# Kernel tuning notes

Measured on AMD Instinct MI355X. Metric: run time of the kernel, lower is better.

The kernel has to match this reference:

```python
import jax, jax.numpy as jnp
import numpy as np

DT_MIN, DT_MAX, STAB_EPS, RMS_EPS = 1e-4, 10.0, 1e-8, 1e-6


def soft_clamp(x, mn=DT_MIN, mx=DT_MAX):
    center = (mx + mn) / 2.0
    half = (mx - mn) / 2.0
    return center + half * jnp.tanh((x - center) / half)


def setup_inputs() -> dict:
    key = jax.random.key(0)
    ks = jax.random.split(key, 8)
    B, L, D, N = 1, 4096, 1024, 16
    s = D ** -0.5
    x = jax.random.normal(ks[0], (B, L, D), jnp.float32)
    # S4D-real style init: A = -exp(A_log), rows = -(1..N)
    A_log = jnp.broadcast_to(jnp.log(jnp.arange(1, N + 1, dtype=jnp.float32)), (D, N))
    W_delta = jax.random.normal(ks[1], (D, D), jnp.float32) * s
    b_delta = jax.random.normal(ks[2], (D,), jnp.float32) * 0.1
    W_B = jax.random.normal(ks[3], (D, N), jnp.float32) * s
    W_C = jax.random.normal(ks[4], (D, N), jnp.float32) * s
    D_skip = jax.random.normal(ks[5], (D,), jnp.float32) * 0.1 + 1.0
    norm_weight = jnp.ones((D,), jnp.float32)
    return {"x": x, "A_log": A_log, "W_delta": W_delta, "b_delta": b_delta,
            "W_B": W_B, "W_C": W_C, "D_skip": D_skip, "norm_weight": norm_weight}


def reference(x, A_log, W_delta, b_delta, W_B, W_C, D_skip, norm_weight):
    # RMSNorm pre-norm
    rms = jnp.sqrt(jnp.mean(x * x, axis=-1, keepdims=True) + RMS_EPS)
    xn = norm_weight * x / rms                                  # (B, L, D)

    # input-dependent (selective) parameters
    delta = soft_clamp(jax.nn.softplus(xn @ W_delta + b_delta))  # (B, L, D)
    Bp = xn @ W_B                                               # (B, L, N)
    C = xn @ W_C                                                # (B, L, N)
    A = -jnp.exp(A_log)                                         # (D, N)

    # guarded Tustin (bilinear) discretization
    half_dA = 0.5 * delta[..., None] * A                        # (B, L, D, N)
    denom_inv = 1.0 / jnp.maximum(1.0 - half_dA, STAB_EPS)
    A_bar = (1.0 + half_dA) * denom_inv                         # (B, L, D, N)
    B_bar = jnp.sqrt(delta)[..., None] * Bp[:, :, None, :] * denom_inv
    Bx = B_bar * xn[..., None]                                  # (B, L, D, N)

    # linear recurrence h_t = A_bar_t * h_{t-1} + Bx_t ; y_t = sum_n C_t * h_t
    def step(h, inp):
        a_t, bx_t, c_t = inp
        h = a_t * h + bx_t                                      # (B, D, N)
        y_t = jnp.einsum('bdn,bn->bd', h, c_t)
        return h, y_t

    h0 = jnp.zeros((x.shape[0], A.shape[0], A.shape[1]), x.dtype)
    seq = (jnp.moveaxis(A_bar, 1, 0), jnp.moveaxis(Bx, 1, 0), jnp.moveaxis(C, 1, 0))
    _, ys = jax.lax.scan(step, h0, seq)
    y = jnp.moveaxis(ys, 0, 1) + D_skip * xn                    # skip connection
    return y
```

## Files before the change

kernel.cpp:

```cpp
#include <hip/hip_runtime.h>
#include <hip/hip_fp16.h>
#include <cmath>

typedef _Float16 half8 __attribute__((ext_vector_type(8)));
typedef _Float16 half4_t __attribute__((ext_vector_type(4)));
typedef float f32x4 __attribute__((ext_vector_type(4)));

#define LDIM 4096
#define DDIM 1024
#define NSTATE 16
#define NCHUNK 128
#define CLEN 32

#define GLD16(g, l) __builtin_amdgcn_global_load_lds( \
    (const __attribute__((address_space(1))) void*)(g), \
    (__attribute__((address_space(3))) void*)(l), 16, 0, 0)

__global__ __launch_bounds__(256) void k_prep_norm(const float* __restrict__ x,
                                                   const float* __restrict__ nw,
                                                   const float* __restrict__ W,
                                                   const float* __restrict__ WB,
                                                   const float* __restrict__ WC,
                                                   _Float16* __restrict__ xnh,
                                                   _Float16* __restrict__ Wt,
                                                   _Float16* __restrict__ BCe) {
  const int b = blockIdx.x, t = threadIdx.x;
  if (b < 4096) {
    const int l = b;
    float4 v = ((const float4*)(x + (size_t)l * DDIM))[t];
    float ss = v.x * v.x + v.y * v.y + v.z * v.z + v.w * v.w;
#pragma unroll
    for (int off = 32; off; off >>= 1) ss += __shfl_xor(ss, off, 64);
    __shared__ float sred[4];
    if ((t & 63) == 0) sred[t >> 6] = ss;
    __syncthreads();
    float tot = sred[0] + sred[1] + sred[2] + sred[3];
    float r = rsqrtf(tot * (1.0f / (float)DDIM) + 1e-6f);
    float4 wv = ((const float4*)nw)[t];
    half4_t h;
    h[0] = (_Float16)(v.x * wv.x * r); h[1] = (_Float16)(v.y * wv.y * r);
    h[2] = (_Float16)(v.z * wv.z * r); h[3] = (_Float16)(v.w * wv.w * r);
    ((half4_t*)(xnh + (size_t)l * DDIM))[t] = h;
  } else if (b < 4352) {
    __shared__ float tile[64][65];
    const int bb = b - 4096;
    const int n0 = (bb & 15) * 64, k0 = (bb >> 4) * 64;
#pragma unroll
    for (int i = 0; i < 16; ++i) {
      int idx = t + i * 256;
      int kk = idx >> 6, nn = idx & 63;
      tile[kk][nn] = W[(size_t)(k0 + kk) * DDIM + n0 + nn];
    }
    __syncthreads();
#pragma unroll
    for (int i = 0; i < 16; ++i) {
      int idx = t + i * 256;
      int nn = idx >> 6, kk = idx & 63;
      Wt[(size_t)(n0 + nn) * DDIM + k0 + kk] = (_Float16)tile[kk][nn];
    }
  } else {
    const int by2 = b - 4352;
#pragma unroll
    for (int rr = 0; rr < 2; ++rr) {
      int r = 2 * by2 + rr;
      const float* src = (r & 1) ? WC : WB;
      int n = r >> 1;
#pragma unroll
      for (int j = 0; j < 4; ++j) {
        int k = t * 4 + j;
        BCe[(size_t)r * DDIM + k] = (_Float16)src[(size_t)k * NSTATE + n];
      }
    }
  }
}

__global__ __launch_bounds__(256, 2) void k_gemm64(const _Float16* __restrict__ Ah,
                                                   const _Float16* __restrict__ Bh,
                                                   const _Float16* __restrict__ B2h,
                                                   const float* __restrict__ b_delta,
                                                   _Float16* __restrict__ sdh,
                                                   float* __restrict__ bpc) {
  __shared__ __align__(16) _Float16 As[2][128 * 64];
  __shared__ __align__(16) _Float16 Bs[2][64 * 64];
  __shared__ __align__(16) _Float16 B2s[2][32 * 64];
  const int t = threadIdx.x;
  const int w = t >> 6, lane = t & 63;
  const int quad = lane >> 4, l16 = lane & 15;
  const int wr = w >> 1, wc = w & 1;
  const int bid = blockIdx.x;
  const int bx = bid & 15, by = bid >> 4;
  const int tileM = by * 128, tileN = bx * 64;
  const int srow = lane >> 3;
  const int sslot = (lane & 7) ^ srow;
  const _Float16* gA0 = Ah + (size_t)(tileM + w * 32 + srow) * DDIM + sslot * 8;
  const _Float16* gB0 = Bh + (size_t)(tileN + w * 16 + srow) * DDIM + sslot * 8;
  const _Float16* gC0 = B2h + (size_t)(w * 8 + srow) * DDIM + sslot * 8;

  f32x4 acc[4][2], acc2[4];
#pragma unroll
  for (int i = 0; i < 4; ++i) {
    acc2[i] = (f32x4){0.f, 0.f, 0.f, 0.f};
#pragma unroll
    for (int j = 0; j < 2; ++j) acc[i][j] = (f32x4){0.f, 0.f, 0.f, 0.f};
  }

  auto stage = [&](int kt, int p) {
    const int ko = kt * 64;
#pragma unroll
    for (int g = 0; g < 4; ++g)
      GLD16(gA0 + (size_t)g * 8 * DDIM + ko, &As[p][(w * 32 + g * 8) * 64]);
#pragma unroll
    for (int g = 0; g < 2; ++g)
      GLD16(gB0 + (size_t)g * 8 * DDIM + ko, &Bs[p][(w * 16 + g * 8) * 64]);
    if (bx == 0)
      GLD16(gC0 + ko, &B2s[p][(w * 8) * 64]);
  };

  stage(0, 0);
  for (int kt = 0; kt < 16; ++kt) {
    const int p = kt & 1;
    __syncthreads();
    if (kt < 15) stage(kt + 1, p ^ 1);
#pragma unroll
    for (int ks = 0; ks < 2; ++ks) {
      const int sw = ((ks * 4 + quad) ^ (l16 & 7)) * 8;
      half8 af[4], bf[2];
#pragma unroll
      for (int i = 0; i < 4; ++i)
        af[i] = *(const half8*)&As[p][(wr * 64 + i * 16 + l16) * 64 + sw];
#pragma unroll
      for (int j = 0; j < 2; ++j)
        bf[j] = *(const half8*)&Bs[p][(wc * 32 + j * 16 + l16) * 64 + sw];
#pragma unroll
      for (int i = 0; i < 4; ++i)
#pragma unroll
        for (int j = 0; j < 2; ++j)
          acc[i][j] = __builtin_amdgcn_mfma_f32_16x16x32_f16(af[i], bf[j], acc[i][j], 0, 0, 0);
      if (bx == 0) {
        half8 cf = *(const half8*)&B2s[p][(wc * 16 + l16) * 64 + sw];
#pragma unroll
        for (int i = 0; i < 4; ++i)
          acc2[i] = __builtin_amdgcn_mfma_f32_16x16x32_f16(af[i], cf, acc2[i], 0, 0, 0);
      }
    }
  }

  const float cC = 5.00005f, cH = 4.99995f, invH = 1.0f / 4.99995f;
  float bdl[2];
#pragma unroll
  for (int j = 0; j < 2; ++j) bdl[j] = b_delta[tileN + wc * 32 + j * 16 + l16];
#pragma unroll
  for (int i = 0; i < 4; ++i) {
#pragma unroll
    for (int r = 0; r < 4; ++r) {
      int row = tileM + wr * 64 + i * 16 + quad * 4 + r;
#pragma unroll
      for (int j = 0; j < 2; ++j) {
        int col = tileN + wc * 32 + j * 16 + l16;
        float z = acc[i][j][r] + bdl[j];
        float e = __expf(-fabsf(z));
        float sp = fmaxf(z, 0.f) + __logf(1.0f + e);
        float tt = (sp - cC) * invH;
        float e2 = __expf(-2.0f * fabsf(tt));
        float th = copysignf((1.0f - e2) / (1.0f + e2), tt);
        float dt = fmaf(cH, th, cC);
        sdh[(size_t)row * DDIM + col] = (_Float16)sqrtf(dt);
      }
      if (bx == 0)
        bpc[(size_t)row * 32 + wc * 16 + l16] = acc2[i][r];
    }
  }
}

__global__ __launch_bounds__(256) void k_scan1(const _Float16* __restrict__ sdh,
                                               const _Float16* __restrict__ xnh,
                                               const float* __restrict__ bpc,
                                               const float* __restrict__ A_log,
                                               float2* __restrict__ Ph) {
  __shared__ float2 bcs[CLEN * NSTATE];
  const int t = threadIdx.x;
  const int d = blockIdx.x * 256 + t;
  const int c = blockIdx.y;
#pragma unroll
  for (int u = t; u < CLEN * NSTATE; u += 256) {
    int l = u >> 4, n2 = (u & 15) * 2;
    bcs[u] = *(const float2*)&bpc[(size_t)(c * CLEN + l) * 32 + n2];
  }
  float halfA[NSTATE], h[NSTATE], P[NSTATE];
#pragma unroll
  for (int n = 0; n < NSTATE; ++n) {
    halfA[n] = -0.5f * __expf(A_log[d * NSTATE + n]);
    h[n] = 0.f; P[n] = 1.f;
  }
  __syncthreads();
  const _Float16* sdr = sdh + (size_t)c * CLEN * DDIM + d;
  const _Float16* xr = xnh + (size_t)c * CLEN * DDIM + d;
#pragma unroll 2
  for (int i = 0; i < CLEN; ++i) {
    float sdv = (float)sdr[(size_t)i * DDIM];
    float xv = (float)xr[(size_t)i * DDIM];
    float dsq = sdv * sdv;
    float sdx = sdv * xv;
#pragma unroll
    for (int n = 0; n < NSTATE; ++n) {
      float2 bc = bcs[i * NSTATE + n];
      float hd = dsq * halfA[n];
      float di = __builtin_amdgcn_rcpf(1.0f - hd);
      float ab = fmaf(hd, di, di);
      h[n] = fmaf(ab, h[n], sdx * bc.x * di);
      P[n] *= ab;
    }
  }
#pragma unroll
  for (int n = 0; n < NSTATE; ++n)
    Ph[((size_t)c * NSTATE + n) * DDIM + d] = make_float2(P[n], h[n]);
}

__global__ __launch_bounds__(64) void k_comb(const float2* __restrict__ Ph,
                                             float* __restrict__ Hinit) {
  const int g = blockIdx.x * 64 + threadIdx.x;
  float H = 0.f;
  for (int cb = 0; cb < NCHUNK; cb += 8) {
    float2 ph[8];
#pragma unroll
    for (int u = 0; u < 8; ++u)
      ph[u] = Ph[(size_t)(cb + u) * (DDIM * NSTATE) + g];
#pragma unroll
    for (int u = 0; u < 8; ++u) {
      Hinit[(size_t)(cb + u) * (DDIM * NSTATE) + g] = H;
      H = fmaf(ph[u].x, H, ph[u].y);
    }
  }
}

__global__ __launch_bounds__(256) void k_scan2(const _Float16* __restrict__ sdh,
                                               const _Float16* __restrict__ xnh,
                                               const float* __restrict__ bpc,
                                               const float* __restrict__ A_log,
                                               const float* __restrict__ Hinit,
                                               const float* __restrict__ Dskip,
                                               float* __restrict__ y) {
  __shared__ float2 bcs[CLEN * NSTATE];
  const int t = threadIdx.x;
  const int d = blockIdx.x * 256 + t;
  const int c = blockIdx.y;
#pragma unroll
  for (int u = t; u < CLEN * NSTATE; u += 256) {
    int l = u >> 4, n2 = (u & 15) * 2;
    bcs[u] = *(const float2*)&bpc[(size_t)(c * CLEN + l) * 32 + n2];
  }
  float halfA[NSTATE], h[NSTATE];
#pragma unroll
  for (int n = 0; n < NSTATE; ++n) {
    halfA[n] = -0.5f * __expf(A_log[d * NSTATE + n]);
    h[n] = Hinit[(size_t)c * (DDIM * NSTATE) + n * DDIM + d];
  }
  const float dsk = Dskip[d];
  __syncthreads();
  const _Float16* sdr = sdh + (size_t)c * CLEN * DDIM + d;
  const _Float16* xr = xnh + (size_t)c * CLEN * DDIM + d;
  float* yr = y + (size_t)c * CLEN * DDIM + d;
#pragma unroll 2
  for (int i = 0; i < CLEN; ++i) {
    float sdv = (float)sdr[(size_t)i * DDIM];
    float xv = (float)xr[(size_t)i * DDIM];
    float dsq = sdv * sdv;
    float sdx = sdv * xv;
    float acc = dsk * xv;
#pragma unroll
    for (int n = 0; n < NSTATE; ++n) {
      float2 bc = bcs[i * NSTATE + n];
      float hd = dsq * halfA[n];
      float di = __builtin_amdgcn_rcpf(1.0f - hd);
      float ab = fmaf(hd, di, di);
      h[n] = fmaf(ab, h[n], sdx * bc.x * di);
      acc = fmaf(bc.y, h[n], acc);
    }
    yr[(size_t)i * DDIM] = acc;
  }
}

extern "C" void kernel_launch(void* const* d_in, const int* in_sizes, int n_in,
                              void* d_out, int out_size, void* d_ws, size_t ws_size,
                              hipStream_t stream) {
  const float* x       = (const float*)d_in[0];
  const float* A_log   = (const float*)d_in[1];
  const float* W_delta = (const float*)d_in[2];
  const float* b_delta = (const float*)d_in[3];
  const float* W_B     = (const float*)d_in[4];
  const float* W_C     = (const float*)d_in[5];
  const float* D_skip  = (const float*)d_in[6];
  const float* norm_w  = (const float*)d_in[7];
  float* y = (float*)d_out;

  char* ws = (char*)d_ws;
  const size_t MB = 1024 * 1024;
  _Float16* xnh = (_Float16*)(ws);
  _Float16* Wt  = (_Float16*)(ws + 8 * MB);
  _Float16* BCe = (_Float16*)(ws + 10 * MB);
  _Float16* sdh = (_Float16*)(ws + 11 * MB);
  float*    bpc = (float*)(ws + 19 * MB);
  float2*   Ph  = (float2*)(ws + 20 * MB);
  float*    Hin = (float*)(ws + 36 * MB);
  (void)ws_size; (void)in_sizes; (void)n_in; (void)out_size;

  hipLaunchKernelGGL(k_prep_norm, dim3(4368), dim3(256), 0, stream,
                     x, norm_w, W_delta, W_B, W_C, xnh, Wt, BCe);
  hipLaunchKernelGGL(k_gemm64, dim3(512), dim3(256), 0, stream,
                     xnh, Wt, BCe, b_delta, sdh, bpc);
  hipLaunchKernelGGL(k_scan1, dim3(4, NCHUNK), dim3(256), 0, stream,
                     sdh, xnh, bpc, A_log, Ph);
  hipLaunchKernelGGL(k_comb, dim3(256), dim3(64), 0, stream, Ph, Hin);
  hipLaunchKernelGGL(k_scan2, dim3(4, NCHUNK), dim3(256), 0, stream,
                     sdh, xnh, bpc, A_log, Hin, D_skip, y);
}
```

Baseline: 160.8 us.

## Pack delta and xn into half2, vectorize scan math, read B/C params uniformly

The GEMM epilogue now writes sqrt(delta) interleaved with the normalized input as a half2 array, so the scan kernels make one 4-byte load per step instead of two 2-byte loads. B and C projections are regrouped into contiguous blocks of 16 and read directly from global memory as uniform addresses, replacing the LDS staging and its barrier. The recurrence uses 2-wide float vectors to allow packed FMA, with A_bar rewritten as 2*di-1. The tanh uses a single exp and a reciprocal, and the chunk-combine unroll goes from 8 to 16. Costs: the epilogue rereads xn, the workspace is laid out differently, and the new tanh form may overflow to inf, though it stays finite.

```diff
diff --git a/kernel.cpp b/kernel.cpp
--- a/kernel.cpp
+++ b/kernel.cpp
@@ -4,7 +4,9 @@
 
 typedef _Float16 half8 __attribute__((ext_vector_type(8)));
 typedef _Float16 half4_t __attribute__((ext_vector_type(4)));
+typedef _Float16 half2_t __attribute__((ext_vector_type(2)));
 typedef float f32x4 __attribute__((ext_vector_type(4)));
+typedef float f32x2 __attribute__((ext_vector_type(2)));
 
 #define LDIM 4096
 #define DDIM 1024
@@ -63,8 +65,8 @@
 #pragma unroll
     for (int rr = 0; rr < 2; ++rr) {
       int r = 2 * by2 + rr;
-      const float* src = (r & 1) ? WC : WB;
-      int n = r >> 1;
+      const float* src = (r < 16) ? WB : WC;
+      int n = r & 15;
 #pragma unroll
       for (int j = 0; j < 4; ++j) {
         int k = t * 4 + j;
@@ -78,7 +80,7 @@
                                                    const _Float16* __restrict__ Bh,
                                                    const _Float16* __restrict__ B2h,
                                                    const float* __restrict__ b_delta,
-                                                   _Float16* __restrict__ sdh,
+                                                   half2_t* __restrict__ sxh,
                                                    float* __restrict__ bpc) {
   __shared__ __align__(16) _Float16 As[2][128 * 64];
   __shared__ __align__(16) _Float16 Bs[2][64 * 64];
@@ -161,10 +163,13 @@
         float e = __expf(-fabsf(z));
         float sp = fmaxf(z, 0.f) + __logf(1.0f + e);
         float tt = (sp - cC) * invH;
-        float e2 = __expf(-2.0f * fabsf(tt));
-        float th = copysignf((1.0f - e2) / (1.0f + e2), tt);
+        float e2 = __expf(2.0f * tt);
+        float th = 1.0f - 2.0f * __builtin_amdgcn_rcpf(e2 + 1.0f);
         float dt = fmaf(cH, th, cC);
-        sdh[(size_t)row * DDIM + col] = (_Float16)sqrtf(dt);
+        half2_t pk;
+        pk[0] = (_Float16)sqrtf(dt);
+        pk[1] = Ah[(size_t)row * DDIM + col];
+        sxh[(size_t)row * DDIM + col] = pk;
       }
       if (bx == 0)
         bpc[(size_t)row * 32 + wc * 16 + l16] = acc2[i][r];
@@ -172,111 +177,114 @@
   }
 }
 
-__global__ __launch_bounds__(256) void k_scan1(const _Float16* __restrict__ sdh,
-                                               const _Float16* __restrict__ xnh,
+__global__ __launch_bounds__(256) void k_scan1(const half2_t* __restrict__ sxh,
                                                const float* __restrict__ bpc,
                                                const float* __restrict__ A_log,
                                                float2* __restrict__ Ph) {
-  __shared__ float2 bcs[CLEN * NSTATE];
   const int t = threadIdx.x;
   const int d = blockIdx.x * 256 + t;
   const int c = blockIdx.y;
-#pragma unroll
-  for (int u = t; u < CLEN * NSTATE; u += 256) {
-    int l = u >> 4, n2 = (u & 15) * 2;
-    bcs[u] = *(const float2*)&bpc[(size_t)(c * CLEN + l) * 32 + n2];
-  }
-  float halfA[NSTATE], h[NSTATE], P[NSTATE];
-#pragma unroll
-  for (int n = 0; n < NSTATE; ++n) {
-    halfA[n] = -0.5f * __expf(A_log[d * NSTATE + n]);
-    h[n] = 0.f; P[n] = 1.f;
-  }
-  __syncthreads();
-  const _Float16* sdr = sdh + (size_t)c * CLEN * DDIM + d;
-  const _Float16* xr = xnh + (size_t)c * CLEN * DDIM + d;
-#pragma unroll 2
+  const float4* alp = (const float4*)(A_log + (size_t)d * NSTATE);
+  f32x2 halfA[8], h[8], P[8];
+#pragma unroll
+  for (int q = 0; q < 4; ++q) {
+    float4 al = alp[q];
+    halfA[2 * q + 0] = (f32x2){-0.5f * __expf(al.x), -0.5f * __expf(al.y)};
+    halfA[2 * q + 1] = (f32x2){-0.5f * __expf(al.z), -0.5f * __expf(al.w)};
+  }
+#pragma unroll
+  for (int j = 0; j < 8; ++j) { h[j] = (f32x2){0.f, 0.f}; P[j] = (f32x2){1.f, 1.f}; }
+  const half2_t* sxr = sxh + (size_t)c * CLEN * DDIM + d;
+  const float* bp0 = bpc + (size_t)c * CLEN * 32;
+  const f32x2 one2 = {1.f, 1.f}, two2 = {2.f, 2.f}, mone2 = {-1.f, -1.f};
+#pragma unroll 4
   for (int i = 0; i < CLEN; ++i) {
-    float sdv = (float)sdr[(size_t)i * DDIM];
-    float xv = (float)xr[(size_t)i * DDIM];
-    float dsq = sdv * sdv;
-    float sdx = sdv * xv;
-#pragma unroll
-    for (int n = 0; n < NSTATE; ++n) {
-      float2 bc = bcs[i * NSTATE + n];
-      float hd = dsq * halfA[n];
-      float di = __builtin_amdgcn_rcpf(1.0f - hd);
-      float ab = fmaf(hd, di, di);
-      h[n] = fmaf(ab, h[n], sdx * bc.x * di);
-      P[n] *= ab;
-    }
-  }
-#pragma unroll
-  for (int n = 0; n < NSTATE; ++n)
-    Ph[((size_t)c * NSTATE + n) * DDIM + d] = make_float2(P[n], h[n]);
+    half2_t sx = sxr[(size_t)i * DDIM];
+    float sdv = (float)sx[0], xv = (float)sx[1];
+    float dsq = sdv * sdv, sdx = sdv * xv;
+    f32x2 dsq2 = {dsq, dsq}, sdx2 = {sdx, sdx};
+    const float* bp = bp0 + i * 32;
+#pragma unroll
+    for (int j = 0; j < 8; ++j) {
+      f32x2 bB = *(const f32x2*)(bp + 2 * j);
+      f32x2 hd = dsq2 * halfA[j];
+      f32x2 om = one2 - hd;
+      f32x2 di = {__builtin_amdgcn_rcpf(om[0]), __builtin_amdgcn_rcpf(om[1])};
+      f32x2 ab = __builtin_elementwise_fma(di, two2, mone2);
+      h[j] = __builtin_elementwise_fma(ab, h[j], sdx2 * bB * di);
+      P[j] = P[j] * ab;
+    }
+  }
+#pragma unroll
+  for (int j = 0; j < 8; ++j) {
+    Ph[((size_t)c * NSTATE + 2 * j + 0) * DDIM + d] = make_float2(P[j][0], h[j][0]);
+    Ph[((size_t)c * NSTATE + 2 * j + 1) * DDIM + d] = make_float2(P[j][1], h[j][1]);
+  }
 }
 
 __global__ __launch_bounds__(64) void k_comb(const float2* __restrict__ Ph,
                                              float* __restrict__ Hinit) {
   const int g = blockIdx.x * 64 + threadIdx.x;
   float H = 0.f;
-  for (int cb = 0; cb < NCHUNK; cb += 8) {
-    float2 ph[8];
-#pragma unroll
-    for (int u = 0; u < 8; ++u)
+  for (int cb = 0; cb < NCHUNK; cb += 16) {
+    float2 ph[16];
+#pragma unroll
+    for (int u = 0; u < 16; ++u)
       ph[u] = Ph[(size_t)(cb + u) * (DDIM * NSTATE) + g];
 #pragma unroll
-    for (int u = 0; u < 8; ++u) {
+    for (int u = 0; u < 16; ++u) {
       Hinit[(size_t)(cb + u) * (DDIM * NSTATE) + g] = H;
       H = fmaf(ph[u].x, H, ph[u].y);
     }
   }
 }
 
-__global__ __launch_bounds__(256) void k_scan2(const _Float16* __restrict__ sdh,
-                                               const _Float16* __restrict__ xnh,
+__global__ __launch_bounds__(256) void k_scan2(const half2_t* __restrict__ sxh,
                                                const float* __restrict__ bpc,
                                                const float* __restrict__ A_log,
                                                const float* __restrict__ Hinit,
                                                const float* __restrict__ Dskip,
                                                float* __restrict__ y) {
-  __shared__ float2 bcs[CLEN * NSTATE];
   const int t = threadIdx.x;
   const int d = blockIdx.x * 256 + t;
   const int c = blockIdx.y;
-#pragma unroll
-  for (int u = t; u < CLEN * NSTATE; u += 256) {
-    int l = u >> 4, n2 = (u & 15) * 2;
-    bcs[u] = *(const float2*)&bpc[(size_t)(c * CLEN + l) * 32 + n2];
-  }
-  float halfA[NSTATE], h[NSTATE];
-#pragma unroll
-  for (int n = 0; n < NSTATE; ++n) {
-    halfA[n] = -0.5f * __expf(A_log[d * NSTATE + n]);
-    h[n] = Hinit[(size_t)c * (DDIM * NSTATE) + n * DDIM + d];
-  }
+  const float4* alp = (const float4*)(A_log + (size_t)d * NSTATE);
+  f32x2 halfA[8], h[8];
+#pragma unroll
+  for (int q = 0; q < 4; ++q) {
+    float4 al = alp[q];
+    halfA[2 * q + 0] = (f32x2){-0.5f * __expf(al.x), -0.5f * __expf(al.y)};
+    halfA[2 * q + 1] = (f32x2){-0.5f * __expf(al.z), -0.5f * __expf(al.w)};
+  }
+#pragma unroll
+  for (int j = 0; j < 8; ++j)
+    h[j] = (f32x2){Hinit[(size_t)c * (DDIM * NSTATE) + (size_t)(2 * j) * DDIM + d],
+                   Hinit[(size_t)c * (DDIM * NSTATE) + (size_t)(2 * j + 1) * DDIM + d]};
   const float dsk = Dskip[d];
-  __syncthreads();
-  const _Float16* sdr = sdh + (size_t)c * CLEN * DDIM + d;
-  const _Float16* xr = xnh + (size_t)c * CLEN * DDIM + d;
+  const half2_t* sxr = sxh + (size_t)c * CLEN * DDIM + d;
+  const float* bp0 = bpc + (size_t)c * CLEN * 32;
   float* yr = y + (size_t)c * CLEN * DDIM + d;
-#pragma unroll 2
+  const f32x2 one2 = {1.f, 1.f}, two2 = {2.f, 2.f}, mone2 = {-1.f, -1.f};
+#pragma unroll 4
   for (int i = 0; i < CLEN; ++i) {
-    float sdv = (float)sdr[(size_t)i * DDIM];
-    float xv = (float)xr[(size_t)i * DDIM];
-    float dsq = sdv * sdv;
-    float sdx = sdv * xv;
-    float acc = dsk * xv;
-#pragma unroll
-    for (int n = 0; n < NSTATE; ++n) {
-      float2 bc = bcs[i * NSTATE + n];
-      float hd = dsq * halfA[n];
-      float di = __builtin_amdgcn_rcpf(1.0f - hd);
-      float ab = fmaf(hd, di, di);
-      h[n] = fmaf(ab, h[n], sdx * bc.x * di);
-      acc = fmaf(bc.y, h[n], acc);
-    }
-    yr[(size_t)i * DDIM] = acc;
+    half2_t sx = sxr[(size_t)i * DDIM];
+    float sdv = (float)sx[0], xv = (float)sx[1];
+    float dsq = sdv * sdv, sdx = sdv * xv;
+    f32x2 dsq2 = {dsq, dsq}, sdx2 = {sdx, sdx};
+    const float* bp = bp0 + i * 32;
+    f32x2 acc = {0.f, 0.f};
+#pragma unroll
+    for (int j = 0; j < 8; ++j) {
+      f32x2 bB = *(const f32x2*)(bp + 2 * j);
+      f32x2 bC = *(const f32x2*)(bp + 16 + 2 * j);
+      f32x2 hd = dsq2 * halfA[j];
+      f32x2 om = one2 - hd;
+      f32x2 di = {__builtin_amdgcn_rcpf(om[0]), __builtin_amdgcn_rcpf(om[1])};
+      f32x2 ab = __builtin_elementwise_fma(di, two2, mone2);
+      h[j] = __builtin_elementwise_fma(ab, h[j], sdx2 * bB * di);
+      acc = __builtin_elementwise_fma(bC, h[j], acc);
+    }
+    yr[(size_t)i * DDIM] = fmaf(dsk, xv, acc[0] + acc[1]);
   }
 }
 
@@ -298,19 +306,19 @@
   _Float16* xnh = (_Float16*)(ws);
   _Float16* Wt  = (_Float16*)(ws + 8 * MB);
   _Float16* BCe = (_Float16*)(ws + 10 * MB);
-  _Float16* sdh = (_Float16*)(ws + 11 * MB);
-  float*    bpc = (float*)(ws + 19 * MB);
-  float2*   Ph  = (float2*)(ws + 20 * MB);
-  float*    Hin = (float*)(ws + 36 * MB);
+  float*    bpc = (float*)(ws + 10 * MB + 512 * 1024);
+  half2_t*  sxh = (half2_t*)(ws + 11 * MB);
+  float2*   Ph  = (float2*)(ws + 27 * MB);
+  float*    Hin = (float*)(ws + 43 * MB);
   (void)ws_size; (void)in_sizes; (void)n_in; (void)out_size;
 
   hipLaunchKernelGGL(k_prep_norm, dim3(4368), dim3(256), 0, stream,
                      x, norm_w, W_delta, W_B, W_C, xnh, Wt, BCe);
   hipLaunchKernelGGL(k_gemm64, dim3(512), dim3(256), 0, stream,
-                     xnh, Wt, BCe, b_delta, sdh, bpc);
+                     xnh, Wt, BCe, b_delta, sxh, bpc);
   hipLaunchKernelGGL(k_scan1, dim3(4, NCHUNK), dim3(256), 0, stream,
-                     sdh, xnh, bpc, A_log, Ph);
+                     sxh, bpc, A_log, Ph);
   hipLaunchKernelGGL(k_comb, dim3(256), dim3(64), 0, stream, Ph, Hin);
   hipLaunchKernelGGL(k_scan2, dim3(4, NCHUNK), dim3(256), 0, stream,
-                     sdh, xnh, bpc, A_log, Hin, D_skip, y);
-}
+                     sxh, bpc, A_log, Hin, D_skip, y);
+}
```

Result: no change. 159.5 us (median of 2 runs) (-0.8%).
